# Performance work log

Hardware: AMD Instinct MI355X
Metric: run time of the kernel (lower is better)

Reference implementation:

```python
import jax, jax.numpy as jnp
import numpy as np

EPS = 1e-10  # faithful to original: masked scores are set to eps, not -inf


def setup_inputs() -> dict:
    key = jax.random.key(0)
    ks = jax.random.split(key, 5)
    B, S, D, N, H = 2, 2048, 1024, 16, 64
    init_range = 0.02
    residual = jax.random.normal(ks[0], (B, S, D), dtype=jnp.float32)
    W_key = jax.random.normal(ks[1], (N, D, H), dtype=jnp.float32) * init_range
    W_query = jax.random.normal(ks[2], (N, D, H), dtype=jnp.float32) * init_range
    W_values = jax.random.normal(ks[3], (N, D, H), dtype=jnp.float32) * init_range
    W_output = jax.random.normal(ks[4], (N, H, D), dtype=jnp.float32) * init_range
    return {
        "residual": residual,
        "W_key": W_key, "W_query": W_query, "W_values": W_values, "W_output": W_output,
        "Bias_key": jnp.zeros((N, H), jnp.float32),
        "Bias_query": jnp.zeros((N, H), jnp.float32),
        "Bias_values": jnp.zeros((N, H), jnp.float32),
        "Bias_output": jnp.zeros((D,), jnp.float32),
    }


def reference(residual, W_key, W_query, W_values, W_output,
              Bias_key, Bias_query, Bias_values, Bias_output):
    B, S, D = residual.shape
    N, _, H = W_key.shape
    # projections: [b,s,n,h]
    keys = jnp.einsum('bse,neh->bsnh', residual, W_key) + Bias_key
    queries = jnp.einsum('bse,neh->bsnh', residual, W_query) + Bias_query
    values = jnp.einsum('bse,neh->bsnh', residual, W_values) + Bias_values
    # scores: [b,n,q,k]
    scores = jnp.einsum('bknh,bqnh->bnqk', keys, queries) / jnp.sqrt(jnp.asarray(H, scores_dtype(residual)))
    q_idx = jnp.arange(S)[:, None]
    k_idx = jnp.arange(S)[None, :]
    causal_mask = q_idx < k_idx  # future positions
    # QUIRK of original module: masked scores are assigned eps (~0), not -inf
    scores = jnp.where(causal_mask[None, None, :, :], jnp.asarray(EPS, scores.dtype), scores)
    probs = jax.nn.softmax(scores, axis=3)
    weighted = jnp.einsum('bnqk,bknh->bqnh', probs, values)
    out = jnp.einsum('bqnh,nhe->bqe', weighted, W_output) + Bias_output
    return out


def scores_dtype(x):
    return x.dtype
```

## Files before the change

kernel.cpp:

```cpp
#include <hip/hip_runtime.h>
#include <hip/hip_bf16.h>
#include <cmath>

typedef __bf16 bf16;
typedef __attribute__((ext_vector_type(4))) __bf16 bf16x4;
typedef __attribute__((ext_vector_type(8))) __bf16 bf16x8;
typedef __attribute__((ext_vector_type(4))) float f32x4;

#define B_ 2
#define S_ 2048
#define D_ 1024
#define N_ 16
#define H_ 64
#define LOG2E 1.44269504088896340736f

__device__ __forceinline__ void gload16(const bf16* g, bf16* l) {
  __builtin_amdgcn_global_load_lds(
      (const __attribute__((address_space(1))) void*)(g),
      (__attribute__((address_space(3))) void*)(l), 16, 0, 0);
}

__device__ __forceinline__ f32x4 mfma16(bf16x8 a, bf16x8 b, f32x4 c) {
  return __builtin_amdgcn_mfma_f32_16x16x32_bf16(a, b, c, 0, 0, 0);
}

__device__ __forceinline__ f32x4 zero4() {
  f32x4 v = {0.0f, 0.0f, 0.0f, 0.0f};
  return v;
}

__global__ __launch_bounds__(256) void cvt_kernel(
    const float* __restrict__ in, bf16* __restrict__ out, int n8) {
  int id = blockIdx.x * 256 + threadIdx.x;
  if (id >= n8) return;
  const float4* p = (const float4*)(in + (size_t)id * 8);
  float4 v0 = p[0], v1 = p[1];
  bf16x8 o;
  o[0] = (bf16)v0.x; o[1] = (bf16)v0.y; o[2] = (bf16)v0.z; o[3] = (bf16)v0.w;
  o[4] = (bf16)v1.x; o[5] = (bf16)v1.y; o[6] = (bf16)v1.z; o[7] = (bf16)v1.w;
  *(bf16x8*)(out + (size_t)id * 8) = o;
}

__global__ __launch_bounds__(256) void qkvw_transpose_kernel(
    const float* __restrict__ Wk, const float* __restrict__ Wq,
    const float* __restrict__ Wv, bf16* __restrict__ out) {
  __shared__ bf16 t[64][72];
  const int z = blockIdx.z;
  const float* W = (z < 16) ? Wk : (z < 32) ? Wq : Wv;
  const float* ing = W + (size_t)(z & 15) * (1024 * 64);
  bf16* outg = out + (size_t)z * (64 * 1024);
  const int r0 = blockIdx.x * 64;
  const int t8 = threadIdx.x & 7, trow = threadIdx.x >> 3;
#pragma unroll
  for (int p = 0; p < 2; ++p) {
    int r = trow + p * 32;
    const float4* src = (const float4*)(ing + (size_t)(r0 + r) * 64 + t8 * 8);
    float4 v0 = src[0], v1 = src[1];
    bf16x8 o;
    o[0] = (bf16)v0.x; o[1] = (bf16)v0.y; o[2] = (bf16)v0.z; o[3] = (bf16)v0.w;
    o[4] = (bf16)v1.x; o[5] = (bf16)v1.y; o[6] = (bf16)v1.z; o[7] = (bf16)v1.w;
    *(bf16x8*)(&t[r][t8 * 8]) = o;
  }
  __syncthreads();
#pragma unroll
  for (int p = 0; p < 2; ++p) {
    int c = trow + p * 32;
    bf16x8 v;
#pragma unroll
    for (int j = 0; j < 8; ++j) v[j] = t[t8 * 8 + j][c];
    *(bf16x8*)(outg + (size_t)c * 1024 + r0 + t8 * 8) = v;
  }
}

__global__ __launch_bounds__(256) void transpose_f32bf16_kernel(
    const float* __restrict__ in, bf16* __restrict__ out, int R, int C) {
  __shared__ bf16 t[64][72];
  const size_t mat = (size_t)R * C;
  const float* ing = in + (size_t)blockIdx.z * mat;
  bf16* outg = out + (size_t)blockIdx.z * mat;
  const int r0 = blockIdx.x * 64, c0 = blockIdx.y * 64;
  const int t8 = threadIdx.x & 7, trow = threadIdx.x >> 3;
#pragma unroll
  for (int p = 0; p < 2; ++p) {
    int r = trow + p * 32;
    const float4* src = (const float4*)(ing + (size_t)(r0 + r) * C + c0 + t8 * 8);
    float4 v0 = src[0], v1 = src[1];
    bf16x8 o;
    o[0] = (bf16)v0.x; o[1] = (bf16)v0.y; o[2] = (bf16)v0.z; o[3] = (bf16)v0.w;
    o[4] = (bf16)v1.x; o[5] = (bf16)v1.y; o[6] = (bf16)v1.z; o[7] = (bf16)v1.w;
    *(bf16x8*)(&t[r][t8 * 8]) = o;
  }
  __syncthreads();
#pragma unroll
  for (int p = 0; p < 2; ++p) {
    int c = trow + p * 32;
    bf16x8 v;
#pragma unroll
    for (int j = 0; j < 8; ++j) v[j] = t[t8 * 8 + j][c];
    *(bf16x8*)(outg + (size_t)(c0 + c) * R + r0 + t8 * 8) = v;
  }
}

__global__ __launch_bounds__(256) void transpose_bf16_kernel(
    const bf16* __restrict__ in, bf16* __restrict__ out, int R, int C) {
  __shared__ bf16 t[64][72];
  const size_t mat = (size_t)R * C;
  const bf16* ing = in + (size_t)blockIdx.z * mat;
  bf16* outg = out + (size_t)blockIdx.z * mat;
  const int r0 = blockIdx.x * 64, c0 = blockIdx.y * 64;
  const int t8 = threadIdx.x & 7, trow = threadIdx.x >> 3;
#pragma unroll
  for (int p = 0; p < 2; ++p) {
    int r = trow + p * 32;
    bf16x8 v = *(const bf16x8*)(ing + (size_t)(r0 + r) * C + c0 + t8 * 8);
    *(bf16x8*)(&t[r][t8 * 8]) = v;
  }
  __syncthreads();
#pragma unroll
  for (int p = 0; p < 2; ++p) {
    int c = trow + p * 32;
    bf16x8 v;
#pragma unroll
    for (int j = 0; j < 8; ++j) v[j] = t[t8 * 8 + j][c];
    *(bf16x8*)(outg + (size_t)(c0 + c) * R + r0 + t8 * 8) = v;
  }
}

__global__ __launch_bounds__(256) void sufv_tot_kernel(
    const bf16* __restrict__ Vp, float* __restrict__ tot) {
  __shared__ float red[4][64];
  const int hd = blockIdx.x, seg = blockIdx.y;
  const int h = threadIdx.x & 63, sub = threadIdx.x >> 6;
  const bf16* Vh = Vp + (size_t)hd * S_ * H_;
  float a = 0.0f;
  const int k0 = seg * 32 + sub * 8;
#pragma unroll
  for (int k = 0; k < 8; ++k) a += (float)Vh[(size_t)(k0 + k) * H_ + h];
  red[sub][h] = a;
  __syncthreads();
  if (sub == 0)
    tot[(hd * 64 + seg) * 64 + h] = red[0][h] + red[1][h] + red[2][h] + red[3][h];
}

__global__ __launch_bounds__(64) void sufv_scan_kernel(
    bf16* __restrict__ VS, const float* __restrict__ tot) {
  const int hd = blockIdx.x, seg = blockIdx.y, h = threadIdx.x;
  bf16* Vh = VS + (size_t)hd * S_ * H_;
  float a = 0.0f;
  for (int s2 = seg + 1; s2 < 64; ++s2) a += tot[(hd * 64 + s2) * 64 + h];
  for (int k = seg * 32 + 31; k >= seg * 32; --k) {
    const float v = (float)Vh[(size_t)k * H_ + h];
    Vh[(size_t)k * H_ + h] = (bf16)a;
    a += v;
  }
}

__global__ __launch_bounds__(256) void gemm_proj_kernel(
    const bf16* __restrict__ A, const bf16* __restrict__ Wt_base,
    const float* __restrict__ bk, const float* __restrict__ bq,
    const float* __restrict__ bv, bf16* __restrict__ proj_base) {
  __shared__ bf16 As[128 * 64];
  __shared__ bf16 Bs[128 * 64];
  const int z = blockIdx.z;
  const bf16* Bt = Wt_base + (size_t)z * (1024 * 1024);
  const float* bias = (z == 0) ? bk : (z == 1 ? bq : bv);
  bf16* Out = proj_base + (size_t)z * ((size_t)B_ * N_ * S_ * H_);
  const int tid = threadIdx.x;
  const int w = tid >> 6, l = tid & 63, lan = l & 15, grp = l >> 4;
  const int mb = (w >> 1) * 64, nb = (w & 1) * 64;
  const int m0 = blockIdx.y * 128, n0 = blockIdx.x * 128;
  const int lrow8 = l >> 3;
  const int swl = ((l & 7) ^ lrow8) * 8;
  const int l7 = lan & 7;

  f32x4 acc[4][4];
#pragma unroll
  for (int i = 0; i < 4; ++i)
#pragma unroll
    for (int j = 0; j < 4; ++j) acc[i][j] = zero4();

  for (int kb = 0; kb < 1024; kb += 64) {
    __syncthreads();
#pragma unroll
    for (int i = 0; i < 4; ++i) {
      int ch = w * 4 + i;
      gload16(A + (size_t)(m0 + ch * 8 + lrow8) * 1024 + kb + swl, As + ch * 512);
      gload16(Bt + (size_t)(n0 + ch * 8 + lrow8) * 1024 + kb + swl, Bs + ch * 512);
    }
    __syncthreads();
#pragma unroll
    for (int kk = 0; kk < 2; ++kk) {
      bf16x8 a[4], b[4];
#pragma unroll
      for (int mf = 0; mf < 4; ++mf)
        a[mf] = *(const bf16x8*)(As + (mb + mf * 16 + lan) * 64 + (((grp + kk * 4) ^ l7) << 3));
#pragma unroll
      for (int nf = 0; nf < 4; ++nf)
        b[nf] = *(const bf16x8*)(Bs + (nb + nf * 16 + lan) * 64 + (((grp + kk * 4) ^ l7) << 3));
#pragma unroll
      for (int mf = 0; mf < 4; ++mf)
#pragma unroll
        for (int nf = 0; nf < 4; ++nf)
          acc[mf][nf] = mfma16(a[mf], b[nf], acc[mf][nf]);
    }
  }
#pragma unroll
  for (int nf = 0; nf < 4; ++nf) {
    int c = n0 + nb + nf * 16 + lan;
    float bs = bias[c];
    int n = c >> 6, h = c & 63;
#pragma unroll
    for (int mf = 0; mf < 4; ++mf) {
#pragma unroll
      for (int r = 0; r < 4; ++r) {
        int m = m0 + mb + mf * 16 + grp * 4 + r;
        int b = m >> 11, s = m & 2047;
        Out[((size_t)((b * N_ + n) * S_ + s)) * H_ + h] = (bf16)(acc[mf][nf][r] + bs);
      }
    }
  }
}

__global__ __launch_bounds__(256) void gemm_out_kernel(
    const bf16* __restrict__ A, const bf16* __restrict__ Bt,
    const float* __restrict__ bias, float* __restrict__ Out) {
  __shared__ bf16 As[128 * 64];
  __shared__ bf16 Bs[128 * 64];
  const int tid = threadIdx.x;
  const int w = tid >> 6, l = tid & 63, lan = l & 15, grp = l >> 4;
  const int mb = (w >> 1) * 64, nb = (w & 1) * 64;
  const int m0 = blockIdx.y * 128, n0 = blockIdx.x * 128;
  const int lrow8 = l >> 3;
  const int swl = ((l & 7) ^ lrow8) * 8;
  const int l7 = lan & 7;

  f32x4 acc[4][4];
#pragma unroll
  for (int i = 0; i < 4; ++i)
#pragma unroll
    for (int j = 0; j < 4; ++j) acc[i][j] = zero4();

  for (int kb = 0; kb < 1024; kb += 64) {
    __syncthreads();
#pragma unroll
    for (int i = 0; i < 4; ++i) {
      int ch = w * 4 + i;
      gload16(A + (size_t)(m0 + ch * 8 + lrow8) * 1024 + kb + swl, As + ch * 512);
      gload16(Bt + (size_t)(n0 + ch * 8 + lrow8) * 1024 + kb + swl, Bs + ch * 512);
    }
    __syncthreads();
#pragma unroll
    for (int kk = 0; kk < 2; ++kk) {
      bf16x8 a[4], b[4];
#pragma unroll
      for (int mf = 0; mf < 4; ++mf)
        a[mf] = *(const bf16x8*)(As + (mb + mf * 16 + lan) * 64 + (((grp + kk * 4) ^ l7) << 3));
#pragma unroll
      for (int nf = 0; nf < 4; ++nf)
        b[nf] = *(const bf16x8*)(Bs + (nb + nf * 16 + lan) * 64 + (((grp + kk * 4) ^ l7) << 3));
#pragma unroll
      for (int mf = 0; mf < 4; ++mf)
#pragma unroll
        for (int nf = 0; nf < 4; ++nf)
          acc[mf][nf] = mfma16(a[mf], b[nf], acc[mf][nf]);
    }
  }
#pragma unroll
  for (int nf = 0; nf < 4; ++nf) {
    int c = n0 + nb + nf * 16 + lan;
    float bs = bias[c];
#pragma unroll
    for (int mf = 0; mf < 4; ++mf) {
#pragma unroll
      for (int r = 0; r < 4; ++r) {
        int m = m0 + mb + mf * 16 + grp * 4 + r;
        Out[(size_t)m * 1024 + c] = acc[mf][nf][r] + bs;
      }
    }
  }
}

__global__ __launch_bounds__(256) void attn_kernel(
    const bf16* __restrict__ Qp, const bf16* __restrict__ Kp,
    const bf16* __restrict__ Vt, const bf16* __restrict__ Suf,
    bf16* __restrict__ Wtd, float* __restrict__ PoA, float* __restrict__ PoB,
    float* __restrict__ PpA, float* __restrict__ PpB) {
  __shared__ bf16 Ks[2][64 * 64];
  __shared__ bf16 Vs[2][64 * 64];
  __shared__ bf16 Ps[4][32 * 72];
  const int tid = threadIdx.x;
  const int w = tid >> 6, l = tid & 63, lan = l & 15, grp = l >> 4;
  const int bi = blockIdx.x;
  const int qq = bi >> 8;
  const int j = bi & 255;
  const int hd = j & 31, wv = j >> 5;
  int x, t0, t1;
  if (qq == 0)      { x = 15 - wv; t0 = 0;     t1 = x + 1; }
  else if (qq == 1) { x = 15 - wv; t0 = x + 1; t1 = 2 * x + 2; }
  else              { x = wv;      t0 = 0;     t1 = 2 * x + 2; }
  const int qw = x * 128 + w * 32;
  const bf16* Qh = Qp + (size_t)hd * S_ * H_;
  const bf16* Kh = Kp + (size_t)hd * S_ * H_;
  const bf16* Vh = Vt + (size_t)hd * H_ * S_;
  const bf16* Sufh = Suf + (size_t)hd * S_ * H_;
  const int lrow8 = l >> 3;
  const int swl = ((l & 7) ^ lrow8) * 8;
  const int l7 = lan & 7;
  const float cexp = 0.125f * LOG2E;

#define STAGE(buf, kb_)                                                        \
  do {                                                                         \
    _Pragma("unroll") for (int i2 = 0; i2 < 2; ++i2) {                         \
      int ch = w * 2 + i2;                                                     \
      gload16(Kh + (size_t)((kb_) + ch * 8 + lrow8) * H_ + swl,                \
              &Ks[buf][ch * 512]);                                             \
      gload16(Vh + (size_t)(ch * 8 + lrow8) * S_ + (kb_) + swl,                \
              &Vs[buf][ch * 512]);                                             \
    }                                                                          \
  } while (0)

  bf16x8 qa[2][2];
#pragma unroll
  for (int qt = 0; qt < 2; ++qt)
#pragma unroll
    for (int kf = 0; kf < 2; ++kf)
      qa[qt][kf] = *(const bf16x8*)(Qh + (size_t)(qw + qt * 16 + lan) * H_ + grp * 8 + kf * 32);

  f32x4 o[2][4];
  float psum[2] = {0.0f, 0.0f};
#pragma unroll
  for (int qt = 0; qt < 2; ++qt)
#pragma unroll
    for (int hf = 0; hf < 4; ++hf) o[qt][hf] = zero4();

  bf16* Pw = &Ps[w][0];

  STAGE(0, t0 * 64);
  for (int tt = t0; tt < t1; ++tt) {
    const int kb = tt * 64;
    const int cur = (tt - t0) & 1;
    if (tt + 1 < t1) {
      STAGE(cur ^ 1, kb + 64);
      asm volatile("s_waitcnt vmcnt(4)" ::: "memory");
    } else {
      asm volatile("s_waitcnt vmcnt(0)" ::: "memory");
    }
    __builtin_amdgcn_s_barrier();

    if (kb <= qw + 31) {
      const bf16* Kc = &Ks[cur][0];
      const bf16* Vc = &Vs[cur][0];

      f32x4 s2[4][2];
#pragma unroll
      for (int k2 = 0; k2 < 4; ++k2)
#pragma unroll
        for (int qt = 0; qt < 2; ++qt) s2[k2][qt] = zero4();
      __builtin_amdgcn_s_setprio(1);
#pragma unroll
      for (int kf = 0; kf < 2; ++kf) {
        bf16x8 kfr[4];
#pragma unroll
        for (int k2 = 0; k2 < 4; ++k2)
          kfr[k2] = *(const bf16x8*)(Kc + (k2 * 16 + lan) * 64 + (((grp + kf * 4) ^ l7) << 3));
#pragma unroll
        for (int k2 = 0; k2 < 4; ++k2)
#pragma unroll
          for (int qt = 0; qt < 2; ++qt)
            s2[k2][qt] = mfma16(kfr[k2], qa[qt][kf], s2[k2][qt]);
      }
      __builtin_amdgcn_s_setprio(0);

      const bool maskt = (kb + 63 > qw);
#pragma unroll
      for (int qt = 0; qt < 2; ++qt) {
        const int q_g = qw + qt * 16 + lan;
#pragma unroll
        for (int k2 = 0; k2 < 4; ++k2) {
          f32x4 p;
#pragma unroll
          for (int r = 0; r < 4; ++r) p[r] = exp2f(s2[k2][qt][r] * cexp);
          if (maskt) {
            const int kg0 = kb + k2 * 16 + grp * 4;
#pragma unroll
            for (int r = 0; r < 4; ++r)
              if (kg0 + r > q_g) p[r] = 0.0f;
          }
          psum[qt] += (p[0] + p[1]) + (p[2] + p[3]);
          unsigned plo, phi;
          asm("v_cvt_pk_bf16_f32 %0, %1, %2" : "=v"(plo) : "v"(p[0]), "v"(p[1]));
          asm("v_cvt_pk_bf16_f32 %0, %1, %2" : "=v"(phi) : "v"(p[2]), "v"(p[3]));
          uint2 u; u.x = plo; u.y = phi;
          *(uint2*)(Pw + (qt * 16 + lan) * 72 + k2 * 16 + grp * 4) = u;
        }
      }

      __builtin_amdgcn_s_setprio(1);
#pragma unroll
      for (int ks = 0; ks < 2; ++ks) {
        bf16x8 pa[2], vb[4];
#pragma unroll
        for (int qt = 0; qt < 2; ++qt)
          pa[qt] = *(const bf16x8*)(Pw + (qt * 16 + lan) * 72 + grp * 8 + ks * 32);
#pragma unroll
        for (int hf = 0; hf < 4; ++hf)
          vb[hf] = *(const bf16x8*)(Vc + (hf * 16 + lan) * 64 + (((grp + ks * 4) ^ l7) << 3));
#pragma unroll
        for (int qt = 0; qt < 2; ++qt)
#pragma unroll
          for (int hf = 0; hf < 4; ++hf)
            o[qt][hf] = mfma16(pa[qt], vb[hf], o[qt][hf]);
      }
      __builtin_amdgcn_s_setprio(0);
    }
    __builtin_amdgcn_s_barrier();
  }
#undef STAGE

#pragma unroll
  for (int qt = 0; qt < 2; ++qt) {
    psum[qt] += __shfl_xor(psum[qt], 16);
    psum[qt] += __shfl_xor(psum[qt], 32);
  }

  if (qq == 2) {
    const size_t outbase = (size_t)(hd >> 4) * S_ * (N_ * H_) + (size_t)(hd & 15) * H_;
#pragma unroll
    for (int qt = 0; qt < 2; ++qt) {
#pragma unroll
      for (int r = 0; r < 4; ++r) {
        const int q_g = qw + qt * 16 + grp * 4 + r;
        const float ps = __shfl(psum[qt], grp * 4 + r);
        const float inv = 1.0f / (ps + (float)(2047 - q_g));
#pragma unroll
        for (int hf = 0; hf < 4; ++hf) {
          const int h = hf * 16 + lan;
          const float suf = (float)Sufh[(size_t)q_g * H_ + h];
          Wtd[outbase + (size_t)q_g * (N_ * H_) + h] = (bf16)((o[qt][hf][r] + suf) * inv);
        }
      }
    }
  } else {
    float* Po = (qq == 0) ? PoA : PoB;
    float* Pp = (qq == 0) ? PpA : PpB;
    const int pb = (hd * 8 + (x - 8)) * 128 + w * 32;
#pragma unroll
    for (int qt = 0; qt < 2; ++qt) {
#pragma unroll
      for (int r = 0; r < 4; ++r) {
        const int rl = qt * 16 + grp * 4 + r;
        const float ps = __shfl(psum[qt], grp * 4 + r);
        if (lan == 0) Pp[pb + rl] = ps;
#pragma unroll
        for (int hf = 0; hf < 4; ++hf)
          Po[(size_t)(pb + rl) * 64 + hf * 16 + lan] = o[qt][hf][r];
      }
    }
  }
}

__global__ __launch_bounds__(256) void combine_kernel(
    const float* __restrict__ PoA, const float* __restrict__ PoB,
    const float* __restrict__ PpA, const float* __restrict__ PpB,
    const bf16* __restrict__ Suf, bf16* __restrict__ Wtd) {
  const int hd = blockIdx.x >> 3, xi = blockIdx.x & 7;
  const int x = xi + 8;
  const int pb = (hd * 8 + xi) * 128;
  const size_t outbase = (size_t)(hd >> 4) * S_ * (N_ * H_) + (size_t)(hd & 15) * H_;
#pragma unroll
  for (int it = 0; it < 8; ++it) {
    const int e = it * 256 + threadIdx.x;
    const int rl = e >> 4, h4 = (e & 15) * 4;
    const int q_g = x * 128 + rl;
    const float Z = PpA[pb + rl] + PpB[pb + rl] + (float)(2047 - q_g);
    const float inv = 1.0f / Z;
    const float4 a = *(const float4*)(PoA + (size_t)(pb + rl) * 64 + h4);
    const float4 b = *(const float4*)(PoB + (size_t)(pb + rl) * 64 + h4);
    const bf16x4 s4 = *(const bf16x4*)(Suf + ((size_t)hd * S_ + q_g) * 64 + h4);
    bf16x4 ov;
    ov[0] = (bf16)((a.x + b.x + (float)s4[0]) * inv);
    ov[1] = (bf16)((a.y + b.y + (float)s4[1]) * inv);
    ov[2] = (bf16)((a.z + b.z + (float)s4[2]) * inv);
    ov[3] = (bf16)((a.w + b.w + (float)s4[3]) * inv);
    *(bf16x4*)(Wtd + outbase + (size_t)q_g * (N_ * H_) + h4) = ov;
  }
}

extern "C" void kernel_launch(void* const* d_in, const int* in_sizes, int n_in,
                              void* d_out, int out_size, void* d_ws, size_t ws_size,
                              hipStream_t stream) {
  const float* residual = (const float*)d_in[0];
  const float* Wk = (const float*)d_in[1];
  const float* Wq = (const float*)d_in[2];
  const float* Wv = (const float*)d_in[3];
  const float* Wo = (const float*)d_in[4];
  const float* Bk = (const float*)d_in[5];
  const float* Bq = (const float*)d_in[6];
  const float* Bv = (const float*)d_in[7];
  const float* Bo = (const float*)d_in[8];
  float* outp = (float*)d_out;

  char* ws = (char*)d_ws;
  const size_t MB = 1024 * 1024;
  bf16* Abf = (bf16*)(ws + 0 * MB);
  bf16* Wot = (bf16*)(ws + 8 * MB);
  bf16* Wkt = (bf16*)(ws + 10 * MB);
  bf16* Kp  = (bf16*)(ws + 16 * MB);
  bf16* Qp  = (bf16*)(ws + 24 * MB);
  bf16* Vp  = (bf16*)(ws + 32 * MB);
  bf16* Vtp = (bf16*)(ws + 40 * MB);
  bf16* Wtd = Abf;
  float* PpA = (float*)(ws + 10 * MB);
  float* PpB = (float*)(ws + 10 * MB + 128 * 1024);
  float* tot = (float*)(ws + 10 * MB + 256 * 1024);
  bf16* Suf = Vp;
  float* PoA = (float*)d_out;
  float* PoB = (float*)d_out + 2 * 1024 * 1024;
  (void)in_sizes; (void)n_in; (void)out_size; (void)ws_size;

  cvt_kernel<<<2048, 256, 0, stream>>>(residual, Abf, (B_ * S_ * D_) / 8);

  qkvw_transpose_kernel<<<dim3(16, 1, 48), 256, 0, stream>>>(Wk, Wq, Wv, Wkt);
  transpose_f32bf16_kernel<<<dim3(16, 16, 1), 256, 0, stream>>>(Wo, Wot, 1024, 1024);

  gemm_proj_kernel<<<dim3(8, 32, 3), 256, 0, stream>>>(Abf, Wkt, Bk, Bq, Bv, Kp);

  sufv_tot_kernel<<<dim3(32, 64), 256, 0, stream>>>(Vp, tot);
  transpose_bf16_kernel<<<dim3(32, 1, 32), 256, 0, stream>>>(Vp, Vtp, 2048, 64);
  sufv_scan_kernel<<<dim3(32, 64), 64, 0, stream>>>(Vp, tot);

  attn_kernel<<<768, 256, 0, stream>>>(Qp, Kp, Vtp, Suf, Wtd, PoA, PoB, PpA, PpB);

  combine_kernel<<<256, 256, 0, stream>>>(PoA, PoB, PpA, PpB, Suf, Wtd);

  gemm_out_kernel<<<dim3(8, 32, 1), 256, 0, stream>>>(Wtd, Wot, Bo, outp);
}
```

Baseline: 158.6 us.

## Fold softmax scale into Q projection, compute row sums via MFMA, restructure staging

Multiplies Q by 0.125*log2e in the projection epilogue so the attention loop calls exp2 on raw scores without a per-element multiply. Row sums of the probabilities are now taken with an extra MFMA against a ones vector, which also covers the bf16-rounded P values, replacing scalar adds and the cross-lane shuffles. The pipeline now issues the next tile's prefetch after a full vmcnt(0) wait and barrier, and drops the trailing barrier. This gives up some load/compute overlap in exchange for one fewer barrier per iteration, and rounding Q to bf16 after scaling changes precision slightly.

```diff
diff --git a/kernel.cpp b/kernel.cpp
--- a/kernel.cpp
+++ b/kernel.cpp
@@ -12,7 +12,7 @@
 #define D_ 1024
 #define N_ 16
 #define H_ 64
-#define LOG2E 1.44269504088896340736f
+#define QSCALE 0.18033688011112042f
 
 __device__ __forceinline__ void gload16(const bf16* g, bf16* l) {
   __builtin_amdgcn_global_load_lds(
@@ -164,6 +164,7 @@
   const int z = blockIdx.z;
   const bf16* Bt = Wt_base + (size_t)z * (1024 * 1024);
   const float* bias = (z == 0) ? bk : (z == 1 ? bq : bv);
+  const float osc = (z == 1) ? QSCALE : 1.0f;
   bf16* Out = proj_base + (size_t)z * ((size_t)B_ * N_ * S_ * H_);
   const int tid = threadIdx.x;
   const int w = tid >> 6, l = tid & 63, lan = l & 15, grp = l >> 4;
@@ -215,7 +216,7 @@
       for (int r = 0; r < 4; ++r) {
         int m = m0 + mb + mf * 16 + grp * 4 + r;
         int b = m >> 11, s = m & 2047;
-        Out[((size_t)((b * N_ + n) * S_ + s)) * H_ + h] = (bf16)(acc[mf][nf][r] + bs);
+        Out[((size_t)((b * N_ + n) * S_ + s)) * H_ + h] = (bf16)((acc[mf][nf][r] + bs) * osc);
       }
     }
   }
@@ -306,7 +307,9 @@
   const int lrow8 = l >> 3;
   const int swl = ((l & 7) ^ lrow8) * 8;
   const int l7 = lan & 7;
-  const float cexp = 0.125f * LOG2E;
+  bf16x8 vones;
+#pragma unroll
+  for (int i = 0; i < 8; ++i) vones[i] = (bf16)1.0f;
 
 #define STAGE(buf, kb_)                                                        \
   do {                                                                         \
@@ -327,11 +330,13 @@
       qa[qt][kf] = *(const bf16x8*)(Qh + (size_t)(qw + qt * 16 + lan) * H_ + grp * 8 + kf * 32);
 
   f32x4 o[2][4];
-  float psum[2] = {0.0f, 0.0f};
-#pragma unroll
-  for (int qt = 0; qt < 2; ++qt)
+  f32x4 psf[2];
+#pragma unroll
+  for (int qt = 0; qt < 2; ++qt) {
+    psf[qt] = zero4();
 #pragma unroll
     for (int hf = 0; hf < 4; ++hf) o[qt][hf] = zero4();
+  }
 
   bf16* Pw = &Ps[w][0];
 
@@ -339,13 +344,9 @@
   for (int tt = t0; tt < t1; ++tt) {
     const int kb = tt * 64;
     const int cur = (tt - t0) & 1;
-    if (tt + 1 < t1) {
-      STAGE(cur ^ 1, kb + 64);
-      asm volatile("s_waitcnt vmcnt(4)" ::: "memory");
-    } else {
-      asm volatile("s_waitcnt vmcnt(0)" ::: "memory");
-    }
+    asm volatile("s_waitcnt vmcnt(0)" ::: "memory");
     __builtin_amdgcn_s_barrier();
+    if (tt + 1 < t1) STAGE(cur ^ 1, kb + 64);
 
     if (kb <= qw + 31) {
       const bf16* Kc = &Ks[cur][0];
@@ -379,14 +380,13 @@
         for (int k2 = 0; k2 < 4; ++k2) {
           f32x4 p;
 #pragma unroll
-          for (int r = 0; r < 4; ++r) p[r] = exp2f(s2[k2][qt][r] * cexp);
+          for (int r = 0; r < 4; ++r) p[r] = exp2f(s2[k2][qt][r]);
           if (maskt) {
             const int kg0 = kb + k2 * 16 + grp * 4;
 #pragma unroll
             for (int r = 0; r < 4; ++r)
               if (kg0 + r > q_g) p[r] = 0.0f;
           }
-          psum[qt] += (p[0] + p[1]) + (p[2] + p[3]);
           unsigned plo, phi;
           asm("v_cvt_pk_bf16_f32 %0, %1, %2" : "=v"(plo) : "v"(p[0]), "v"(p[1]));
           asm("v_cvt_pk_bf16_f32 %0, %1, %2" : "=v"(phi) : "v"(p[2]), "v"(p[3]));
@@ -406,22 +406,17 @@
         for (int hf = 0; hf < 4; ++hf)
           vb[hf] = *(const bf16x8*)(Vc + (hf * 16 + lan) * 64 + (((grp + ks * 4) ^ l7) << 3));
 #pragma unroll
-        for (int qt = 0; qt < 2; ++qt)
+        for (int qt = 0; qt < 2; ++qt) {
 #pragma unroll
           for (int hf = 0; hf < 4; ++hf)
             o[qt][hf] = mfma16(pa[qt], vb[hf], o[qt][hf]);
+          psf[qt] = mfma16(pa[qt], vones, psf[qt]);
+        }
       }
       __builtin_amdgcn_s_setprio(0);
     }
-    __builtin_amdgcn_s_barrier();
   }
 #undef STAGE
-
-#pragma unroll
-  for (int qt = 0; qt < 2; ++qt) {
-    psum[qt] += __shfl_xor(psum[qt], 16);
-    psum[qt] += __shfl_xor(psum[qt], 32);
-  }
 
   if (qq == 2) {
     const size_t outbase = (size_t)(hd >> 4) * S_ * (N_ * H_) + (size_t)(hd & 15) * H_;
@@ -430,8 +425,7 @@
 #pragma unroll
       for (int r = 0; r < 4; ++r) {
         const int q_g = qw + qt * 16 + grp * 4 + r;
-        const float ps = __shfl(psum[qt], grp * 4 + r);
-        const float inv = 1.0f / (ps + (float)(2047 - q_g));
+        const float inv = 1.0f / (psf[qt][r] + (float)(2047 - q_g));
 #pragma unroll
         for (int hf = 0; hf < 4; ++hf) {
           const int h = hf * 16 + lan;
@@ -449,8 +443,7 @@
 #pragma unroll
       for (int r = 0; r < 4; ++r) {
         const int rl = qt * 16 + grp * 4 + r;
-        const float ps = __shfl(psum[qt], grp * 4 + r);
-        if (lan == 0) Pp[pb + rl] = ps;
+        if (lan == 0) Pp[pb + rl] = psf[qt][r];
 #pragma unroll
         for (int hf = 0; hf < 4; ++hf)
           Po[(size_t)(pb + rl) * 64 + hf * 16 + lan] = o[qt][hf][r];
```

Result: slower. 171.8 us (+8.3%).
